# Kernel tuning notes

Measured on AMD Instinct MI355X. Metric: run time of the kernel, lower is better.

The kernel has to match this reference:

```python
import jax, jax.numpy as jnp
import numpy as np

N = 50000      # nodes per graph
E = 1600000    # edges per graph
D_IN = 128
D_HID = 128
D_OUT = 128
D_GF = 128
N_LAYERS = 3   # input->hid, hid->hid (hidden_layer=1), hid->out


def setup_inputs() -> dict:
    key = jax.random.key(0)
    ks = jax.random.split(key, 24)
    inp = {
        "feat_p": jax.random.normal(ks[0], (N, D_IN), jnp.float32),
        "src_p": jax.random.randint(ks[1], (E,), 0, N, jnp.int32),
        "dst_p": jax.random.randint(ks[2], (E,), 0, N, jnp.int32),
        "feat_s": jax.random.normal(ks[3], (N, D_IN), jnp.float32),
        "src_s": jax.random.randint(ks[4], (E,), 0, N, jnp.int32),
        "dst_s": jax.random.randint(ks[5], (E,), 0, N, jnp.int32),
    }
    dims = [(D_IN, D_HID), (D_HID, D_HID), (D_HID, D_OUT)]
    for i, (di, do) in enumerate(dims):
        inp[f"W{i}"] = jax.random.normal(ks[6 + 2 * i], (di, do), jnp.float32) * 0.05
        inp[f"b{i}"] = jnp.zeros((do,), jnp.float32)
    inp["Wr"] = jax.random.normal(ks[14], (D_OUT, D_GF), jnp.float32) * 0.05
    inp["br"] = jnp.zeros((D_GF,), jnp.float32)
    inp["Wm1"] = jax.random.normal(ks[15], (2 * D_GF, D_GF), jnp.float32) * 0.05
    inp["bm1"] = jnp.zeros((D_GF,), jnp.float32)
    inp["Wm2"] = jax.random.normal(ks[16], (D_GF, 1), jnp.float32) * 0.05
    inp["bm2"] = jnp.zeros((1,), jnp.float32)
    return inp


def _gcn_stack(feat, src, dst, layers):
    """Stacked GCN: mean over incoming messages, then linear.
    NOTE: the original SingleGCN never applies its ReLU (bug preserved)."""
    n = feat.shape[0]
    deg = jax.ops.segment_sum(jnp.ones_like(src, feat.dtype), dst, num_segments=n)
    inv_deg = (1.0 / jnp.maximum(deg, 1.0))[:, None]  # [N,1]
    h = feat
    for W, b in layers:
        msg = h[src]                                           # [E,d] gather
        agg = jax.ops.segment_sum(msg, dst, num_segments=n)    # [N,d] scatter-add
        h = (agg * inv_deg) @ W + b                            # mean + linear
    return h


def reference(feat_p, src_p, dst_p, feat_s, src_s, dst_s,
              W0, b0, W1, b1, W2, b2, Wr, br, Wm1, bm1, Wm2, bm2):
    layers = [(W0, b0), (W1, b1), (W2, b2)]
    h_p = _gcn_stack(feat_p, src_p, dst_p, layers)
    h_s = _gcn_stack(feat_s, src_s, dst_s, layers)
    # ReadOut: mean over nodes -> linear -> sigmoid
    g_p = jax.nn.sigmoid(jnp.mean(h_p, axis=0) @ Wr + br)  # [D_GF]
    g_s = jax.nn.sigmoid(jnp.mean(h_s, axis=0) @ Wr + br)
    # Match: concat -> linear -> linear -> sigmoid
    c = jnp.concatenate([g_p, g_s], axis=-1)               # [2*D_GF]
    d = (c @ Wm1 + bm1) @ Wm2 + bm2                        # [1]
    return jax.nn.sigmoid(d)
```

## Files before the change

kernel.cpp:

```cpp
#include <hip/hip_runtime.h>
#include <math.h>

#define D 128


__global__ __launch_bounds__(512) void scan_scatter(
        const int* __restrict__ tgt_p, const int* __restrict__ oth_p,
        const int* __restrict__ tgt_s, const int* __restrict__ oth_s,
        const float* __restrict__ w, float* __restrict__ rep,
        float* __restrict__ sums,
        int E, int N, int HN, int B, int H, float scale) {
    const int b = blockIdx.x, h = blockIdx.y, g = blockIdx.z;
    const int* tgt = g ? tgt_s : tgt_p;
    const int* oth = g ? oth_s : oth_p;
    const float* wg = w ? (w + (size_t)g * N) : nullptr;

    if (!w && b == 0 && h == 0 && g == 0 && threadIdx.x < 16) sums[threadIdx.x] = 0.f;

    extern __shared__ float lds[];
    {
        float4 z = make_float4(0.f, 0.f, 0.f, 0.f);
        float4* l4 = (float4*)lds;
        for (int i = threadIdx.x; i < HN / 4; i += blockDim.x) l4[i] = z;
    }
    __syncthreads();

    const int lo = h * HN;
    const int hi = min(lo + HN, N);
    const unsigned span = (unsigned)(hi - lo);
    int C = (E + B - 1) / B;
    C = (C + 15) & ~15;
    const int e0 = b * C;
    const int e1 = min(e0 + C, E);

    for (int e = e0 + (int)threadIdx.x * 16; e < e1; e += (int)blockDim.x * 16) {
        if (e + 16 <= e1) {
            int idx[16];
            #pragma unroll
            for (int q = 0; q < 4; ++q) {
                int4 t4 = *(const int4*)(tgt + e + 4 * q);
                idx[4 * q + 0] = t4.x; idx[4 * q + 1] = t4.y;
                idx[4 * q + 2] = t4.z; idx[4 * q + 3] = t4.w;
            }
            bool hit[16];
            #pragma unroll
            for (int k = 0; k < 16; ++k) hit[k] = (unsigned)(idx[k] - lo) < span;
            if (wg) {
                int od[16];
                #pragma unroll
                for (int q = 0; q < 4; ++q) {
                    int4 o4 = *(const int4*)(oth + e + 4 * q);
                    od[4 * q + 0] = o4.x; od[4 * q + 1] = o4.y;
                    od[4 * q + 2] = o4.z; od[4 * q + 3] = o4.w;
                }
                float val[16];
                #pragma unroll
                for (int k = 0; k < 16; ++k) val[k] = hit[k] ? wg[od[k]] : 0.f;
                #pragma unroll
                for (int k = 0; k < 16; ++k)
                    if (hit[k]) atomicAdd(&lds[idx[k] - lo], val[k] * scale);
            } else {
                #pragma unroll
                for (int k = 0; k < 16; ++k)
                    if (hit[k]) atomicAdd(&lds[idx[k] - lo], 1.0f);
            }
        } else {
            for (int e2 = e; e2 < e1; ++e2) {
                int t = tgt[e2];
                if ((unsigned)(t - lo) < span) {
                    float v = wg ? wg[oth[e2]] * scale : 1.0f;
                    atomicAdd(&lds[t - lo], v);
                }
            }
        }
    }
    __syncthreads();

    float* dst = rep + (((size_t)g * H + h) * B + b) * HN;
    float4* d4 = (float4*)dst;
    const float4* l4 = (const float4*)lds;
    for (int i = threadIdx.x; i < HN / 4; i += blockDim.x) d4[i] = l4[i];
}

__global__ __launch_bounds__(256) void reduce_inv(
        const float* __restrict__ rep, float* __restrict__ inv,
        int N, int HN, int H, int B) {
    const int lane = threadIdx.x & 63;
    const int s = threadIdx.x >> 6;
    const int i = (blockIdx.x * 64 + lane) * 4;
    const int bps = B >> 2;
    float4 u = make_float4(0.f, 0.f, 0.f, 0.f);
    if (i < 2 * N) {
        int g = (i < N) ? 0 : 1;
        int n = i - g * N;
        int h = n / HN, l = n - h * HN;
        const float* base = rep + (((size_t)g * H + h) * B + (size_t)s * bps) * HN + l;
        #pragma unroll 24
        for (int b = 0; b < bps; b++) {
            float4 v = *(const float4*)(base + (size_t)b * HN);
            u.x += v.x; u.y += v.y; u.z += v.z; u.w += v.w;
        }
    }
    __shared__ float4 sm[256];
    sm[threadIdx.x] = u;
    __syncthreads();
    if (s == 0 && i < 2 * N) {
        float4 a = sm[lane], b4 = sm[64 + lane], c = sm[128 + lane], d = sm[192 + lane];
        float4 r;
        r.x = 1.0f / fmaxf(a.x + b4.x + c.x + d.x, 1.0f);
        r.y = 1.0f / fmaxf(a.y + b4.y + c.y + d.y, 1.0f);
        r.z = 1.0f / fmaxf(a.z + b4.z + c.z + d.z, 1.0f);
        r.w = 1.0f / fmaxf(a.w + b4.w + c.w + d.w, 1.0f);
        *(float4*)(inv + i) = r;
    }
}

__global__ __launch_bounds__(256) void reduce_u(
        const float* __restrict__ rep, const float* __restrict__ inv,
        float* __restrict__ out_u, float* __restrict__ out_w,
        float* __restrict__ sums, int s_idx, int N, int HN, int H, int B) {
    const int lane = threadIdx.x & 63;
    const int s = threadIdx.x >> 6;
    const int i = (blockIdx.x * 64 + lane) * 4;
    const int bps = B >> 2;
    float4 u = make_float4(0.f, 0.f, 0.f, 0.f);
    if (i < 2 * N) {
        int g = (i < N) ? 0 : 1;
        int n = i - g * N;
        int h = n / HN, l = n - h * HN;
        const float* base = rep + (((size_t)g * H + h) * B + (size_t)s * bps) * HN + l;
        #pragma unroll 24
        for (int b = 0; b < bps; b++) {
            float4 v = *(const float4*)(base + (size_t)b * HN);
            u.x += v.x; u.y += v.y; u.z += v.z; u.w += v.w;
        }
    }
    __shared__ float4 sm[256];
    __shared__ float s0[64], s1[64];
    sm[threadIdx.x] = u;
    __syncthreads();
    if (s == 0) {
        float tp = 0.f, ts = 0.f;
        if (i < 2 * N) {
            float4 a = sm[lane], b4 = sm[64 + lane], c = sm[128 + lane], d = sm[192 + lane];
            float4 uu;
            uu.x = a.x + b4.x + c.x + d.x;
            uu.y = a.y + b4.y + c.y + d.y;
            uu.z = a.z + b4.z + c.z + d.z;
            uu.w = a.w + b4.w + c.w + d.w;
            if (out_u) *(float4*)(out_u + i) = uu;
            if (out_w) {
                float4 iv = *(const float4*)(inv + i);
                *(float4*)(out_w + i) =
                    make_float4(uu.x * iv.x, uu.y * iv.y, uu.z * iv.z, uu.w * iv.w);
            }
            float t = uu.x + uu.y + uu.z + uu.w;
            if (i < N) tp = t; else ts = t;
        }
        s0[lane] = tp; s1[lane] = ts;
    }
    __syncthreads();
    if (sums) {
        for (int st = 32; st > 0; st >>= 1) {
            if ((int)threadIdx.x < st) {
                s0[threadIdx.x] += s0[threadIdx.x + st];
                s1[threadIdx.x] += s1[threadIdx.x + st];
            }
            __syncthreads();
        }
        if (threadIdx.x == 0) {
            if (s0[0] != 0.f) atomicAdd(&sums[0 * 2 + s_idx], s0[0]);
            if (s1[0] != 0.f) atomicAdd(&sums[1 * 2 + s_idx], s1[0]);
        }
    }
}

__global__ __launch_bounds__(256) void featsum_kernel(
        const float* __restrict__ feat_p, const float* __restrict__ feat_s,
        const float* __restrict__ u3, float* __restrict__ fpart, int N, int rpb) {
    const int g = blockIdx.y;
    const float* feat = g ? feat_s : feat_p;
    const float* u = u3 + (size_t)g * N;
    const int nb = gridDim.x;
    const int col4 = threadIdx.x & 31;
    const int rgrp = threadIdx.x >> 5;
    const int r0 = blockIdx.x * rpb;
    const int r1 = min(r0 + rpb, N);

    const float4* f4 = (const float4*)feat;
    float4 acc = make_float4(0.f, 0.f, 0.f, 0.f);
    for (int n = r0 + rgrp * 4; n + 3 < r1; n += 32) {
        float4 uu = *(const float4*)(u + n);
        float4 v0 = f4[(size_t)n * 32 + col4];
        float4 v1 = f4[(size_t)(n + 1) * 32 + col4];
        float4 v2 = f4[(size_t)(n + 2) * 32 + col4];
        float4 v3 = f4[(size_t)(n + 3) * 32 + col4];
        acc.x += uu.x * v0.x + uu.y * v1.x + uu.z * v2.x + uu.w * v3.x;
        acc.y += uu.x * v0.y + uu.y * v1.y + uu.z * v2.y + uu.w * v3.y;
        acc.z += uu.x * v0.z + uu.y * v1.z + uu.z * v2.z + uu.w * v3.z;
        acc.w += uu.x * v0.w + uu.y * v1.w + uu.z * v2.w + uu.w * v3.w;
    }
    __shared__ float4 smem[256];
    smem[threadIdx.x] = acc;
    __syncthreads();
    if (rgrp == 0) {
        float4 t = smem[col4];
        #pragma unroll
        for (int k = 1; k < 8; k++) {
            float4 o = smem[k * 32 + col4];
            t.x += o.x; t.y += o.y; t.z += o.z; t.w += o.w;
        }
        float4* dst = (float4*)(fpart + ((size_t)g * nb + blockIdx.x) * 128);
        dst[col4] = t;
    }
}

__global__ __launch_bounds__(256) void fpart_reduce(
        const float* __restrict__ fpart, float* __restrict__ fpart2, int NB) {
    const int b = blockIdx.x, g = blockIdx.y;
    const int j = threadIdx.x & 127, half = threadIdx.x >> 7;
    const int per = NB / 16;
    const int hp = per / 2;
    const float* fp = fpart + ((size_t)(g * NB + b * per + half * hp)) * 128 + j;
    float s = 0.f;
    #pragma unroll 24
    for (int k = 0; k < hp; ++k) s += fp[(size_t)k * 128];
    __shared__ float sm[2][128];
    sm[half][j] = s;
    __syncthreads();
    if (half == 0) fpart2[((size_t)g * 16 + b) * 128 + j] = sm[0][j] + sm[1][j];
}

__global__ __launch_bounds__(512) void final_kernel(
        const float* __restrict__ fpart2,
        const float* __restrict__ sums,
        const float* __restrict__ W0, const float* __restrict__ b0,
        const float* __restrict__ W1, const float* __restrict__ b1,
        const float* __restrict__ W2, const float* __restrict__ b2,
        const float* __restrict__ Wr, const float* __restrict__ br,
        const float* __restrict__ Wm1, const float* __restrict__ bm1,
        const float* __restrict__ Wm2, const float* __restrict__ bm2,
        float* __restrict__ out) {
    __shared__ float x[128];
    __shared__ float part[4][128];
    __shared__ float rvec[256];
    __shared__ float Avec[128], Bvec[128];
    __shared__ float gv[256];
    const int tid = threadIdx.x;
    const int j = tid & 127;
    const int h = tid >> 7;

    auto mv128 = [&](const float* __restrict__ W, float* __restrict__ buf) {
        float p = 0.f;
        const float* Wp = W + (size_t)(h * 32) * 128 + j;
        #pragma unroll
        for (int i = 0; i < 32; ++i) p += buf[h * 32 + i] * Wp[(size_t)i * 128];
        part[h][j] = p;
        __syncthreads();
        if (h == 0) buf[j] = part[0][j] + part[1][j] + part[2][j] + part[3][j];
        __syncthreads();
    };

    if (tid < 256) {
        int g = tid >> 7;
        const float* fp = fpart2 + (size_t)g * 2048 + (tid & 127);
        float rv = 0.f;
        #pragma unroll
        for (int b = 0; b < 16; ++b) rv += fp[(size_t)b * 128];
        rvec[tid] = rv;
    }
    __syncthreads();

    if (tid < 128) x[tid] = b0[tid];
    __syncthreads();
    mv128(W1, x);
    mv128(W2, x);
    if (tid < 128) Avec[tid] = x[tid];
    __syncthreads();
    if (tid < 128) x[tid] = b1[tid];
    __syncthreads();
    mv128(W2, x);
    if (tid < 128) Bvec[tid] = x[tid];
    __syncthreads();

    for (int g = 0; g < 2; ++g) {
        const float s1 = sums[g * 2 + 0];
        const float s2 = sums[g * 2 + 1];
        if (tid < 128) x[tid] = rvec[g * 128 + tid];
        __syncthreads();
        mv128(W0, x);
        mv128(W1, x);
        mv128(W2, x);
        if (tid < 128) x[tid] += s2 * Avec[tid] + s1 * Bvec[tid] + b2[tid];
        __syncthreads();
        mv128(Wr, x);
        if (tid < 128) gv[g * 128 + tid] = 1.0f / (1.0f + expf(-(x[tid] + br[tid])));
        __syncthreads();
    }

    {
        float p = 0.f;
        const float* Wp = Wm1 + (size_t)(h * 64) * 128 + j;
        #pragma unroll
        for (int i = 0; i < 64; ++i) p += gv[h * 64 + i] * Wp[(size_t)i * 128];
        part[h][j] = p;
        __syncthreads();
        if (h == 0)
            part[0][j] = (part[0][j] + part[1][j] + part[2][j] + part[3][j] + bm1[j]) * Wm2[j];
        __syncthreads();
        if (tid < 64) part[0][tid] += part[0][tid + 64];
        __syncthreads();
        if (tid < 32) part[0][tid] += part[0][tid + 32];
        __syncthreads();
        if (tid < 16) part[0][tid] += part[0][tid + 16];
        __syncthreads();
        if (tid < 8) part[0][tid] += part[0][tid + 8];
        __syncthreads();
        if (tid < 4) part[0][tid] += part[0][tid + 4];
        __syncthreads();
        if (tid < 2) part[0][tid] += part[0][tid + 2];
        __syncthreads();
        if (tid == 0) out[0] = 1.0f / (1.0f + expf(-(part[0][0] + part[0][1] + bm2[0])));
    }
}

extern "C" void kernel_launch(void* const* d_in, const int* in_sizes, int n_in,
                              void* d_out, int out_size, void* d_ws, size_t ws_size,
                              hipStream_t stream) {
    const float* feat_p = (const float*)d_in[0];
    const int*   src_p  = (const int*)d_in[1];
    const int*   dst_p  = (const int*)d_in[2];
    const float* feat_s = (const float*)d_in[3];
    const int*   src_s  = (const int*)d_in[4];
    const int*   dst_s  = (const int*)d_in[5];
    const float* W0 = (const float*)d_in[6];
    const float* b0 = (const float*)d_in[7];
    const float* W1 = (const float*)d_in[8];
    const float* b1 = (const float*)d_in[9];
    const float* W2 = (const float*)d_in[10];
    const float* b2 = (const float*)d_in[11];
    const float* Wr = (const float*)d_in[12];
    const float* br = (const float*)d_in[13];
    const float* Wm1 = (const float*)d_in[14];
    const float* bm1 = (const float*)d_in[15];
    const float* Wm2 = (const float*)d_in[16];
    const float* bm2 = (const float*)d_in[17];
    float* out = (float*)d_out;

    const int N = in_sizes[0] / D;
    const int E = in_sizes[1];
    const int N2 = 2 * N;

    const int H = 4;
    int HN = (N + H - 1) / H;
    HN = (HN + 3) & ~3;
    const int NB = 768;
    int rpb = ((N + NB - 1) / NB + 3) & ~3;

    const size_t head = 16 + 4 * (size_t)N2 + (size_t)2 * NB * 128 + 2 * 16 * 128;
    size_t avail = ws_size / sizeof(float);
    int B = 8;
    if (avail > head) {
        size_t bmax = (avail - head) / ((size_t)2 * H * HN);
        if (bmax > 96) bmax = 96;
        B = (int)(bmax & ~(size_t)7);
        if (B < 8) B = 8;
    }

    float* ws     = (float*)d_ws;
    float* sums   = ws;
    float* inv    = ws + 16;
    float* w1     = inv + N2;
    float* w2     = w1 + N2;
    float* u3     = w2 + N2;
    float* fpart  = u3 + N2;
    float* fpart2 = fpart + (size_t)2 * NB * 128;
    float* rep    = fpart2 + 2 * 16 * 128;

    const int BTS = 512;
    const int BT = 256;
    const dim3 sgrid(B, H, 2);
    const size_t lds_bytes = (size_t)HN * sizeof(float);
    const int gQ = (N2 / 4 + 63) / 64;
    const float u0 = 1.0f / (float)N;

    scan_scatter<<<sgrid, BTS, lds_bytes, stream>>>(dst_p, nullptr, dst_s, nullptr,
                                                    nullptr, rep, sums, E, N, HN, B, H, 1.0f);
    reduce_inv<<<gQ, BT, 0, stream>>>(rep, inv, N, HN, H, B);

    scan_scatter<<<sgrid, BTS, lds_bytes, stream>>>(src_p, dst_p, src_s, dst_s,
                                                    inv, rep, sums, E, N, HN, B, H, u0);
    reduce_u<<<gQ, BT, 0, stream>>>(rep, inv, nullptr, w1, sums, 0, N, HN, H, B);

    scan_scatter<<<sgrid, BTS, lds_bytes, stream>>>(src_p, dst_p, src_s, dst_s,
                                                    w1, rep, sums, E, N, HN, B, H, 1.0f);
    reduce_u<<<gQ, BT, 0, stream>>>(rep, inv, nullptr, w2, sums, 1, N, HN, H, B);

    scan_scatter<<<sgrid, BTS, lds_bytes, stream>>>(src_p, dst_p, src_s, dst_s,
                                                    w2, rep, sums, E, N, HN, B, H, 1.0f);
    reduce_u<<<gQ, BT, 0, stream>>>(rep, inv, u3, nullptr, nullptr, 0, N, HN, H, B);

    featsum_kernel<<<dim3(NB, 2), BT, 0, stream>>>(feat_p, feat_s, u3, fpart, N, rpb);
    fpart_reduce<<<dim3(16, 2), BT, 0, stream>>>(fpart, fpart2, NB);

    final_kernel<<<1, 512, 0, stream>>>(fpart2, sums, W0, b0, W1, b1, W2, b2,
                                        Wr, br, Wm1, bm1, Wm2, bm2, out);
}
```

Measured before the change: 288.8 us.

## Fuse all phases into one persistent kernel with software grid barriers

Replaces the eleven separate kernel launches (scatter passes, reductions, feature sum, final MLP) with a single persistent kernel of 512 blocks that runs each phase and separates phases with atomic-counter grid barriers. It fixes the edge-split count at 64 blocks per partition instead of sizing it from workspace, and resizes the reduction and featsum block mappings. The aim is to remove launch gaps and tail effects between the short phases. In exchange it relies on all 512 blocks being co-resident (deadlock risk otherwise) and adds barrier spin cost plus a memset of the counters.

```diff
diff --git a/kernel.cpp b/kernel.cpp
--- a/kernel.cpp
+++ b/kernel.cpp
@@ -2,38 +2,73 @@
 #include <math.h>
 
 #define D 128
-
-
-__global__ __launch_bounds__(512) void scan_scatter(
-        const int* __restrict__ tgt_p, const int* __restrict__ oth_p,
-        const int* __restrict__ tgt_s, const int* __restrict__ oth_s,
-        const float* __restrict__ w, float* __restrict__ rep,
-        float* __restrict__ sums,
-        int E, int N, int HN, int B, int H, float scale) {
-    const int b = blockIdx.x, h = blockIdx.y, g = blockIdx.z;
+#define HQ 4
+#define NBLK 512
+#define BB 64
+
+
+struct Params {
+    const float* feat_p; const int* src_p; const int* dst_p;
+    const float* feat_s; const int* src_s; const int* dst_s;
+    const float *W0, *b0, *W1, *b1, *W2, *b2;
+    const float *Wr, *br, *Wm1, *bm1, *Wm2, *bm2;
+    float* out;
+    int*   bar;
+    float* sums;
+    float* inv;
+    float* w1;
+    float* w2;
+    float* u3;
+    float* fpart;
+    float* fpart2;
+    float* rep;
+    int N, E, HN, NBg;
+    float u0;
+};
+
+__device__ __forceinline__ void gsync(int* bar, int idx) {
+    __syncthreads();
+    if (threadIdx.x == 0) {
+        __threadfence();
+        atomicAdd(&bar[idx], 1);
+        while (__hip_atomic_load(&bar[idx], __ATOMIC_RELAXED,
+                                 __HIP_MEMORY_SCOPE_AGENT) < NBLK)
+            __builtin_amdgcn_s_sleep(2);
+        __threadfence();
+    }
+    __syncthreads();
+}
+
+__device__ __forceinline__ void scan_phase(
+        const Params& p, float* lds,
+        const int* tgt_p, const int* oth_p,
+        const int* tgt_s, const int* oth_s,
+        const float* w, float scale) {
+    const int HN = p.HN, N = p.N, E = p.E;
+    const int id = blockIdx.x;
+    const int b = id % BB;
+    const int h = (id / BB) % HQ;
+    const int g = id / (HQ * BB);
     const int* tgt = g ? tgt_s : tgt_p;
     const int* oth = g ? oth_s : oth_p;
     const float* wg = w ? (w + (size_t)g * N) : nullptr;
 
-    if (!w && b == 0 && h == 0 && g == 0 && threadIdx.x < 16) sums[threadIdx.x] = 0.f;
-
-    extern __shared__ float lds[];
     {
         float4 z = make_float4(0.f, 0.f, 0.f, 0.f);
         float4* l4 = (float4*)lds;
-        for (int i = threadIdx.x; i < HN / 4; i += blockDim.x) l4[i] = z;
+        for (int i = threadIdx.x; i < HN / 4; i += 512) l4[i] = z;
     }
     __syncthreads();
 
     const int lo = h * HN;
     const int hi = min(lo + HN, N);
     const unsigned span = (unsigned)(hi - lo);
-    int C = (E + B - 1) / B;
+    int C = (E + BB - 1) / BB;
     C = (C + 15) & ~15;
     const int e0 = b * C;
     const int e1 = min(e0 + C, E);
 
-    for (int e = e0 + (int)threadIdx.x * 16; e < e1; e += (int)blockDim.x * 16) {
+    for (int e = e0 + (int)threadIdx.x * 16; e < e1; e += 512 * 16) {
         if (e + 16 <= e1) {
             int idx[16];
             #pragma unroll
@@ -76,92 +111,67 @@
     }
     __syncthreads();
 
-    float* dst = rep + (((size_t)g * H + h) * B + b) * HN;
+    float* dst = p.rep + (((size_t)g * HQ + h) * BB + b) * HN;
     float4* d4 = (float4*)dst;
     const float4* l4 = (const float4*)lds;
-    for (int i = threadIdx.x; i < HN / 4; i += blockDim.x) d4[i] = l4[i];
-}
-
-__global__ __launch_bounds__(256) void reduce_inv(
-        const float* __restrict__ rep, float* __restrict__ inv,
-        int N, int HN, int H, int B) {
-    const int lane = threadIdx.x & 63;
-    const int s = threadIdx.x >> 6;
-    const int i = (blockIdx.x * 64 + lane) * 4;
-    const int bps = B >> 2;
+    for (int i = threadIdx.x; i < HN / 4; i += 512) d4[i] = l4[i];
+}
+
+__device__ __forceinline__ void reduce_phase(
+        const Params& p, float* lds, int mode, int s_idx,
+        float* out_u, float* out_w) {
+    const int N = p.N, HN = p.HN;
+    const int lane = threadIdx.x & 127;
+    const int s = threadIdx.x >> 7;
+    const int i = (blockIdx.x * 128 + lane) * 4;
+    const int bps = BB >> 2;
     float4 u = make_float4(0.f, 0.f, 0.f, 0.f);
     if (i < 2 * N) {
         int g = (i < N) ? 0 : 1;
         int n = i - g * N;
         int h = n / HN, l = n - h * HN;
-        const float* base = rep + (((size_t)g * H + h) * B + (size_t)s * bps) * HN + l;
-        #pragma unroll 24
+        const float* base = p.rep + (((size_t)g * HQ + h) * BB + (size_t)s * bps) * HN + l;
+        #pragma unroll 16
         for (int b = 0; b < bps; b++) {
             float4 v = *(const float4*)(base + (size_t)b * HN);
             u.x += v.x; u.y += v.y; u.z += v.z; u.w += v.w;
         }
     }
-    __shared__ float4 sm[256];
-    sm[threadIdx.x] = u;
-    __syncthreads();
-    if (s == 0 && i < 2 * N) {
-        float4 a = sm[lane], b4 = sm[64 + lane], c = sm[128 + lane], d = sm[192 + lane];
-        float4 r;
-        r.x = 1.0f / fmaxf(a.x + b4.x + c.x + d.x, 1.0f);
-        r.y = 1.0f / fmaxf(a.y + b4.y + c.y + d.y, 1.0f);
-        r.z = 1.0f / fmaxf(a.z + b4.z + c.z + d.z, 1.0f);
-        r.w = 1.0f / fmaxf(a.w + b4.w + c.w + d.w, 1.0f);
-        *(float4*)(inv + i) = r;
-    }
-}
-
-__global__ __launch_bounds__(256) void reduce_u(
-        const float* __restrict__ rep, const float* __restrict__ inv,
-        float* __restrict__ out_u, float* __restrict__ out_w,
-        float* __restrict__ sums, int s_idx, int N, int HN, int H, int B) {
-    const int lane = threadIdx.x & 63;
-    const int s = threadIdx.x >> 6;
-    const int i = (blockIdx.x * 64 + lane) * 4;
-    const int bps = B >> 2;
-    float4 u = make_float4(0.f, 0.f, 0.f, 0.f);
-    if (i < 2 * N) {
-        int g = (i < N) ? 0 : 1;
-        int n = i - g * N;
-        int h = n / HN, l = n - h * HN;
-        const float* base = rep + (((size_t)g * H + h) * B + (size_t)s * bps) * HN + l;
-        #pragma unroll 24
-        for (int b = 0; b < bps; b++) {
-            float4 v = *(const float4*)(base + (size_t)b * HN);
-            u.x += v.x; u.y += v.y; u.z += v.z; u.w += v.w;
-        }
-    }
-    __shared__ float4 sm[256];
-    __shared__ float s0[64], s1[64];
+    float4* sm = (float4*)lds;
+    float* s0 = lds + 2048;
+    float* s1 = lds + 2176;
     sm[threadIdx.x] = u;
     __syncthreads();
     if (s == 0) {
         float tp = 0.f, ts = 0.f;
         if (i < 2 * N) {
-            float4 a = sm[lane], b4 = sm[64 + lane], c = sm[128 + lane], d = sm[192 + lane];
+            float4 a = sm[lane], b4 = sm[128 + lane], c = sm[256 + lane], d = sm[384 + lane];
             float4 uu;
             uu.x = a.x + b4.x + c.x + d.x;
             uu.y = a.y + b4.y + c.y + d.y;
             uu.z = a.z + b4.z + c.z + d.z;
             uu.w = a.w + b4.w + c.w + d.w;
-            if (out_u) *(float4*)(out_u + i) = uu;
-            if (out_w) {
-                float4 iv = *(const float4*)(inv + i);
-                *(float4*)(out_w + i) =
-                    make_float4(uu.x * iv.x, uu.y * iv.y, uu.z * iv.z, uu.w * iv.w);
-            }
-            float t = uu.x + uu.y + uu.z + uu.w;
-            if (i < N) tp = t; else ts = t;
+            if (mode == 0) {
+                float4 r;
+                r.x = 1.0f / fmaxf(uu.x, 1.0f); r.y = 1.0f / fmaxf(uu.y, 1.0f);
+                r.z = 1.0f / fmaxf(uu.z, 1.0f); r.w = 1.0f / fmaxf(uu.w, 1.0f);
+                *(float4*)(p.inv + i) = r;
+            } else {
+                if (out_u) *(float4*)(out_u + i) = uu;
+                if (out_w) {
+                    float4 iv = *(const float4*)(p.inv + i);
+                    *(float4*)(out_w + i) =
+                        make_float4(uu.x * iv.x, uu.y * iv.y, uu.z * iv.z, uu.w * iv.w);
+                }
+                float t = uu.x + uu.y + uu.z + uu.w;
+                if (i < N) tp = t; else ts = t;
+            }
         }
         s0[lane] = tp; s1[lane] = ts;
     }
     __syncthreads();
-    if (sums) {
-        for (int st = 32; st > 0; st >>= 1) {
+    if (mode == 1 && s_idx >= 0) {
+        for (int st = 64; st > 0; st >>= 1) {
             if ((int)threadIdx.x < st) {
                 s0[threadIdx.x] += s0[threadIdx.x + st];
                 s1[threadIdx.x] += s1[threadIdx.x + st];
@@ -169,27 +179,28 @@
             __syncthreads();
         }
         if (threadIdx.x == 0) {
-            if (s0[0] != 0.f) atomicAdd(&sums[0 * 2 + s_idx], s0[0]);
-            if (s1[0] != 0.f) atomicAdd(&sums[1 * 2 + s_idx], s1[0]);
-        }
-    }
-}
-
-__global__ __launch_bounds__(256) void featsum_kernel(
-        const float* __restrict__ feat_p, const float* __restrict__ feat_s,
-        const float* __restrict__ u3, float* __restrict__ fpart, int N, int rpb) {
-    const int g = blockIdx.y;
-    const float* feat = g ? feat_s : feat_p;
-    const float* u = u3 + (size_t)g * N;
-    const int nb = gridDim.x;
+            if (s0[0] != 0.f) atomicAdd(&p.sums[0 * 2 + s_idx], s0[0]);
+            if (s1[0] != 0.f) atomicAdd(&p.sums[1 * 2 + s_idx], s1[0]);
+        }
+    }
+}
+
+__device__ __forceinline__ void featsum_phase(const Params& p, float* lds) {
+    const int NBg = p.NBg;
+    const int id = blockIdx.x;
+    const int g = id / NBg;
+    const int bg = id - g * NBg;
+    const float* feat = g ? p.feat_s : p.feat_p;
+    const float* u = p.u3 + (size_t)g * p.N;
+    const int rpb = ((p.N + NBg - 1) / NBg + 3) & ~3;
+    const int r0 = bg * rpb;
+    const int r1 = min(r0 + rpb, p.N);
     const int col4 = threadIdx.x & 31;
-    const int rgrp = threadIdx.x >> 5;
-    const int r0 = blockIdx.x * rpb;
-    const int r1 = min(r0 + rpb, N);
+    const int rg = threadIdx.x >> 5;
 
     const float4* f4 = (const float4*)feat;
     float4 acc = make_float4(0.f, 0.f, 0.f, 0.f);
-    for (int n = r0 + rgrp * 4; n + 3 < r1; n += 32) {
+    for (int n = r0 + rg * 4; n + 3 < r1; n += 64) {
         float4 uu = *(const float4*)(u + n);
         float4 v0 = f4[(size_t)n * 32 + col4];
         float4 v1 = f4[(size_t)(n + 1) * 32 + col4];
@@ -200,70 +211,63 @@
         acc.z += uu.x * v0.z + uu.y * v1.z + uu.z * v2.z + uu.w * v3.z;
         acc.w += uu.x * v0.w + uu.y * v1.w + uu.z * v2.w + uu.w * v3.w;
     }
-    __shared__ float4 smem[256];
+    float4* smem = (float4*)lds;
     smem[threadIdx.x] = acc;
     __syncthreads();
-    if (rgrp == 0) {
+    if (rg == 0) {
         float4 t = smem[col4];
         #pragma unroll
-        for (int k = 1; k < 8; k++) {
+        for (int k = 1; k < 16; k++) {
             float4 o = smem[k * 32 + col4];
             t.x += o.x; t.y += o.y; t.z += o.z; t.w += o.w;
         }
-        float4* dst = (float4*)(fpart + ((size_t)g * nb + blockIdx.x) * 128);
+        float4* dst = (float4*)(p.fpart + ((size_t)g * NBg + bg) * 128);
         dst[col4] = t;
     }
 }
 
-__global__ __launch_bounds__(256) void fpart_reduce(
-        const float* __restrict__ fpart, float* __restrict__ fpart2, int NB) {
-    const int b = blockIdx.x, g = blockIdx.y;
-    const int j = threadIdx.x & 127, half = threadIdx.x >> 7;
-    const int per = NB / 16;
-    const int hp = per / 2;
-    const float* fp = fpart + ((size_t)(g * NB + b * per + half * hp)) * 128 + j;
+__device__ __forceinline__ void fpart2_phase(const Params& p, float* lds) {
+    if (blockIdx.x >= 32) return;
+    const int g = blockIdx.x >> 4, b = blockIdx.x & 15;
+    const int per = p.NBg / 16;
+    const int sl = per / 4;
+    const int j = threadIdx.x & 127, seg = threadIdx.x >> 7;
+    const float* fp = p.fpart + ((size_t)(g * p.NBg + b * per + seg * sl)) * 128 + j;
     float s = 0.f;
-    #pragma unroll 24
-    for (int k = 0; k < hp; ++k) s += fp[(size_t)k * 128];
-    __shared__ float sm[2][128];
-    sm[half][j] = s;
-    __syncthreads();
-    if (half == 0) fpart2[((size_t)g * 16 + b) * 128 + j] = sm[0][j] + sm[1][j];
-}
-
-__global__ __launch_bounds__(512) void final_kernel(
-        const float* __restrict__ fpart2,
-        const float* __restrict__ sums,
-        const float* __restrict__ W0, const float* __restrict__ b0,
-        const float* __restrict__ W1, const float* __restrict__ b1,
-        const float* __restrict__ W2, const float* __restrict__ b2,
-        const float* __restrict__ Wr, const float* __restrict__ br,
-        const float* __restrict__ Wm1, const float* __restrict__ bm1,
-        const float* __restrict__ Wm2, const float* __restrict__ bm2,
-        float* __restrict__ out) {
-    __shared__ float x[128];
-    __shared__ float part[4][128];
-    __shared__ float rvec[256];
-    __shared__ float Avec[128], Bvec[128];
-    __shared__ float gv[256];
+    #pragma unroll 4
+    for (int k = 0; k < sl; ++k) s += fp[(size_t)k * 128];
+    lds[seg * 128 + j] = s;
+    __syncthreads();
+    if (seg == 0)
+        p.fpart2[((size_t)g * 16 + b) * 128 + j] =
+            lds[j] + lds[128 + j] + lds[256 + j] + lds[384 + j];
+}
+
+__device__ __forceinline__ void final_phase(const Params& p, float* lds) {
+    float* x    = lds;
+    float* part = lds + 128;
+    float* rvec = lds + 640;
+    float* Avec = lds + 896;
+    float* Bvec = lds + 1024;
+    float* gv   = lds + 1152;
     const int tid = threadIdx.x;
     const int j = tid & 127;
     const int h = tid >> 7;
 
     auto mv128 = [&](const float* __restrict__ W, float* __restrict__ buf) {
-        float p = 0.f;
+        float pp = 0.f;
         const float* Wp = W + (size_t)(h * 32) * 128 + j;
         #pragma unroll
-        for (int i = 0; i < 32; ++i) p += buf[h * 32 + i] * Wp[(size_t)i * 128];
-        part[h][j] = p;
-        __syncthreads();
-        if (h == 0) buf[j] = part[0][j] + part[1][j] + part[2][j] + part[3][j];
+        for (int i = 0; i < 32; ++i) pp += buf[h * 32 + i] * Wp[(size_t)i * 128];
+        part[h * 128 + j] = pp;
+        __syncthreads();
+        if (h == 0) buf[j] = part[j] + part[128 + j] + part[256 + j] + part[384 + j];
         __syncthreads();
     };
 
     if (tid < 256) {
         int g = tid >> 7;
-        const float* fp = fpart2 + (size_t)g * 2048 + (tid & 127);
+        const float* fp = p.fpart2 + (size_t)g * 2048 + (tid & 127);
         float rv = 0.f;
         #pragma unroll
         for (int b = 0; b < 16; ++b) rv += fp[(size_t)b * 128];
@@ -271,138 +275,122 @@
     }
     __syncthreads();
 
-    if (tid < 128) x[tid] = b0[tid];
-    __syncthreads();
-    mv128(W1, x);
-    mv128(W2, x);
+    if (tid < 128) x[tid] = p.b0[tid];
+    __syncthreads();
+    mv128(p.W1, x);
+    mv128(p.W2, x);
     if (tid < 128) Avec[tid] = x[tid];
     __syncthreads();
-    if (tid < 128) x[tid] = b1[tid];
-    __syncthreads();
-    mv128(W2, x);
+    if (tid < 128) x[tid] = p.b1[tid];
+    __syncthreads();
+    mv128(p.W2, x);
     if (tid < 128) Bvec[tid] = x[tid];
     __syncthreads();
 
     for (int g = 0; g < 2; ++g) {
-        const float s1 = sums[g * 2 + 0];
-        const float s2 = sums[g * 2 + 1];
+        const float s1 = p.sums[g * 2 + 0];
+        const float s2 = p.sums[g * 2 + 1];
         if (tid < 128) x[tid] = rvec[g * 128 + tid];
         __syncthreads();
-        mv128(W0, x);
-        mv128(W1, x);
-        mv128(W2, x);
-        if (tid < 128) x[tid] += s2 * Avec[tid] + s1 * Bvec[tid] + b2[tid];
-        __syncthreads();
-        mv128(Wr, x);
-        if (tid < 128) gv[g * 128 + tid] = 1.0f / (1.0f + expf(-(x[tid] + br[tid])));
+        mv128(p.W0, x);
+        mv128(p.W1, x);
+        mv128(p.W2, x);
+        if (tid < 128) x[tid] += s2 * Avec[tid] + s1 * Bvec[tid] + p.b2[tid];
+        __syncthreads();
+        mv128(p.Wr, x);
+        if (tid < 128) gv[g * 128 + tid] = 1.0f / (1.0f + expf(-(x[tid] + p.br[tid])));
         __syncthreads();
     }
 
     {
-        float p = 0.f;
-        const float* Wp = Wm1 + (size_t)(h * 64) * 128 + j;
+        float pp = 0.f;
+        const float* Wp = p.Wm1 + (size_t)(h * 64) * 128 + j;
         #pragma unroll
-        for (int i = 0; i < 64; ++i) p += gv[h * 64 + i] * Wp[(size_t)i * 128];
-        part[h][j] = p;
+        for (int i = 0; i < 64; ++i) pp += gv[h * 64 + i] * Wp[(size_t)i * 128];
+        part[h * 128 + j] = pp;
         __syncthreads();
         if (h == 0)
-            part[0][j] = (part[0][j] + part[1][j] + part[2][j] + part[3][j] + bm1[j]) * Wm2[j];
-        __syncthreads();
-        if (tid < 64) part[0][tid] += part[0][tid + 64];
-        __syncthreads();
-        if (tid < 32) part[0][tid] += part[0][tid + 32];
-        __syncthreads();
-        if (tid < 16) part[0][tid] += part[0][tid + 16];
-        __syncthreads();
-        if (tid < 8) part[0][tid] += part[0][tid + 8];
-        __syncthreads();
-        if (tid < 4) part[0][tid] += part[0][tid + 4];
-        __syncthreads();
-        if (tid < 2) part[0][tid] += part[0][tid + 2];
-        __syncthreads();
-        if (tid == 0) out[0] = 1.0f / (1.0f + expf(-(part[0][0] + part[0][1] + bm2[0])));
-    }
+            part[j] = (part[j] + part[128 + j] + part[256 + j] + part[384 + j] + p.bm1[j]) * p.Wm2[j];
+        __syncthreads();
+        for (int st = 64; st > 1; st >>= 1) {
+            if (tid < st) part[tid] += part[tid + st];
+            __syncthreads();
+        }
+        if (tid == 0)
+            p.out[0] = 1.0f / (1.0f + expf(-(part[0] + part[1] + p.bm2[0])));
+    }
+}
+
+__global__ __launch_bounds__(512, 4) void fused_kernel(Params p) {
+    extern __shared__ float lds[];
+    int* bar = p.bar;
+
+    scan_phase(p, lds, p.dst_p, nullptr, p.dst_s, nullptr, nullptr, 1.0f);
+    gsync(bar, 0);
+    reduce_phase(p, lds, 0, -1, nullptr, nullptr);
+    gsync(bar, 1);
+    scan_phase(p, lds, p.src_p, p.dst_p, p.src_s, p.dst_s, p.inv, p.u0);
+    gsync(bar, 2);
+    reduce_phase(p, lds, 1, 0, nullptr, p.w1);
+    gsync(bar, 3);
+    scan_phase(p, lds, p.src_p, p.dst_p, p.src_s, p.dst_s, p.w1, 1.0f);
+    gsync(bar, 4);
+    reduce_phase(p, lds, 1, 1, nullptr, p.w2);
+    gsync(bar, 5);
+    scan_phase(p, lds, p.src_p, p.dst_p, p.src_s, p.dst_s, p.w2, 1.0f);
+    gsync(bar, 6);
+    reduce_phase(p, lds, 1, -1, p.u3, nullptr);
+    gsync(bar, 7);
+    featsum_phase(p, lds);
+    gsync(bar, 8);
+    fpart2_phase(p, lds);
+    gsync(bar, 9);
+    if (blockIdx.x == 0) final_phase(p, lds);
 }
 
 extern "C" void kernel_launch(void* const* d_in, const int* in_sizes, int n_in,
                               void* d_out, int out_size, void* d_ws, size_t ws_size,
                               hipStream_t stream) {
-    const float* feat_p = (const float*)d_in[0];
-    const int*   src_p  = (const int*)d_in[1];
-    const int*   dst_p  = (const int*)d_in[2];
-    const float* feat_s = (const float*)d_in[3];
-    const int*   src_s  = (const int*)d_in[4];
-    const int*   dst_s  = (const int*)d_in[5];
-    const float* W0 = (const float*)d_in[6];
-    const float* b0 = (const float*)d_in[7];
-    const float* W1 = (const float*)d_in[8];
-    const float* b1 = (const float*)d_in[9];
-    const float* W2 = (const float*)d_in[10];
-    const float* b2 = (const float*)d_in[11];
-    const float* Wr = (const float*)d_in[12];
-    const float* br = (const float*)d_in[13];
-    const float* Wm1 = (const float*)d_in[14];
-    const float* bm1 = (const float*)d_in[15];
-    const float* Wm2 = (const float*)d_in[16];
-    const float* bm2 = (const float*)d_in[17];
-    float* out = (float*)d_out;
-
     const int N = in_sizes[0] / D;
     const int E = in_sizes[1];
     const int N2 = 2 * N;
 
-    const int H = 4;
-    int HN = (N + H - 1) / H;
+    int HN = (N + HQ - 1) / HQ;
     HN = (HN + 3) & ~3;
-    const int NB = 768;
-    int rpb = ((N + NB - 1) / NB + 3) & ~3;
-
-    const size_t head = 16 + 4 * (size_t)N2 + (size_t)2 * NB * 128 + 2 * 16 * 128;
-    size_t avail = ws_size / sizeof(float);
-    int B = 8;
-    if (avail > head) {
-        size_t bmax = (avail - head) / ((size_t)2 * H * HN);
-        if (bmax > 96) bmax = 96;
-        B = (int)(bmax & ~(size_t)7);
-        if (B < 8) B = 8;
-    }
+    const int NBg = NBLK / 2;
 
     float* ws     = (float*)d_ws;
-    float* sums   = ws;
-    float* inv    = ws + 16;
+    int*   bar    = (int*)ws;
+    float* sums   = ws + 32;
+    float* inv    = ws + 48;
     float* w1     = inv + N2;
     float* w2     = w1 + N2;
     float* u3     = w2 + N2;
     float* fpart  = u3 + N2;
-    float* fpart2 = fpart + (size_t)2 * NB * 128;
+    float* fpart2 = fpart + (size_t)2 * NBg * 128;
     float* rep    = fpart2 + 2 * 16 * 128;
 
-    const int BTS = 512;
-    const int BT = 256;
-    const dim3 sgrid(B, H, 2);
-    const size_t lds_bytes = (size_t)HN * sizeof(float);
-    const int gQ = (N2 / 4 + 63) / 64;
-    const float u0 = 1.0f / (float)N;
-
-    scan_scatter<<<sgrid, BTS, lds_bytes, stream>>>(dst_p, nullptr, dst_s, nullptr,
-                                                    nullptr, rep, sums, E, N, HN, B, H, 1.0f);
-    reduce_inv<<<gQ, BT, 0, stream>>>(rep, inv, N, HN, H, B);
-
-    scan_scatter<<<sgrid, BTS, lds_bytes, stream>>>(src_p, dst_p, src_s, dst_s,
-                                                    inv, rep, sums, E, N, HN, B, H, u0);
-    reduce_u<<<gQ, BT, 0, stream>>>(rep, inv, nullptr, w1, sums, 0, N, HN, H, B);
-
-    scan_scatter<<<sgrid, BTS, lds_bytes, stream>>>(src_p, dst_p, src_s, dst_s,
-                                                    w1, rep, sums, E, N, HN, B, H, 1.0f);
-    reduce_u<<<gQ, BT, 0, stream>>>(rep, inv, nullptr, w2, sums, 1, N, HN, H, B);
-
-    scan_scatter<<<sgrid, BTS, lds_bytes, stream>>>(src_p, dst_p, src_s, dst_s,
-                                                    w2, rep, sums, E, N, HN, B, H, 1.0f);
-    reduce_u<<<gQ, BT, 0, stream>>>(rep, inv, u3, nullptr, nullptr, 0, N, HN, H, B);
-
-    featsum_kernel<<<dim3(NB, 2), BT, 0, stream>>>(feat_p, feat_s, u3, fpart, N, rpb);
-    fpart_reduce<<<dim3(16, 2), BT, 0, stream>>>(fpart, fpart2, NB);
-
-    final_kernel<<<1, 512, 0, stream>>>(fpart2, sums, W0, b0, W1, b1, W2, b2,
-                                        Wr, br, Wm1, bm1, Wm2, bm2, out);
-}
+    hipMemsetAsync(d_ws, 0, 48 * sizeof(float), stream);
+
+    Params p;
+    p.feat_p = (const float*)d_in[0];
+    p.src_p  = (const int*)d_in[1];
+    p.dst_p  = (const int*)d_in[2];
+    p.feat_s = (const float*)d_in[3];
+    p.src_s  = (const int*)d_in[4];
+    p.dst_s  = (const int*)d_in[5];
+    p.W0 = (const float*)d_in[6];  p.b0 = (const float*)d_in[7];
+    p.W1 = (const float*)d_in[8];  p.b1 = (const float*)d_in[9];
+    p.W2 = (const float*)d_in[10]; p.b2 = (const float*)d_in[11];
+    p.Wr = (const float*)d_in[12]; p.br = (const float*)d_in[13];
+    p.Wm1 = (const float*)d_in[14]; p.bm1 = (const float*)d_in[15];
+    p.Wm2 = (const float*)d_in[16]; p.bm2 = (const float*)d_in[17];
+    p.out = (float*)d_out;
+    p.bar = bar; p.sums = sums; p.inv = inv; p.w1 = w1; p.w2 = w2; p.u3 = u3;
+    p.fpart = fpart; p.fpart2 = fpart2; p.rep = rep;
+    p.N = N; p.E = E; p.HN = HN; p.NBg = NBg;
+    p.u0 = 1.0f / (float)N;
+
+    const unsigned lds_bytes = (unsigned)(HN * sizeof(float));
+    fused_kernel<<<NBLK, 512, lds_bytes, stream>>>(p);
+}
```

After: 889.9 us. 3.08x slower.

## Fix scatter grid, widen blocks to 1024 threads, fold feature partial reduction into atomics

Applied to the files above, without the earlier changes.

The edge-scatter kernel now uses a fixed grid of 64 edge chunks by 4 node ranges by 2 graphs, with 1024-thread blocks each handling 8 edges per thread. Previously the number of chunks was derived from workspace size, up to 96, with 512 threads and 16 edges per thread. The featsum kernel drops from 768 to 256 blocks and accumulates its partials directly into 16 bins with global atomics, which removes the separate fpart_reduce launch. Zeroing of the sums and bins moves into the first scatter launch. The trade-offs are a different amount of replicated LDS output per reduction pass and possible atomic contention on the bins.

```diff
diff --git a/kernel.cpp b/kernel.cpp
--- a/kernel.cpp
+++ b/kernel.cpp
@@ -2,66 +2,61 @@
 #include <math.h>
 
 #define D 128
-
-
-__global__ __launch_bounds__(512) void scan_scatter(
+#define HQ 4
+#define BB 64
+
+
+__global__ __launch_bounds__(1024, 8) void scan_scatter(
         const int* __restrict__ tgt_p, const int* __restrict__ oth_p,
         const int* __restrict__ tgt_s, const int* __restrict__ oth_s,
         const float* __restrict__ w, float* __restrict__ rep,
-        float* __restrict__ sums,
-        int E, int N, int HN, int B, int H, float scale) {
+        float* __restrict__ zbase, int zcount,
+        int E, int N, int HN, float scale) {
     const int b = blockIdx.x, h = blockIdx.y, g = blockIdx.z;
     const int* tgt = g ? tgt_s : tgt_p;
     const int* oth = g ? oth_s : oth_p;
     const float* wg = w ? (w + (size_t)g * N) : nullptr;
 
-    if (!w && b == 0 && h == 0 && g == 0 && threadIdx.x < 16) sums[threadIdx.x] = 0.f;
+    if (zbase && b == 0 && h == 0 && g == 0)
+        for (int i = threadIdx.x; i < zcount; i += 1024) zbase[i] = 0.f;
 
     extern __shared__ float lds[];
     {
         float4 z = make_float4(0.f, 0.f, 0.f, 0.f);
         float4* l4 = (float4*)lds;
-        for (int i = threadIdx.x; i < HN / 4; i += blockDim.x) l4[i] = z;
+        for (int i = threadIdx.x; i < HN / 4; i += 1024) l4[i] = z;
     }
     __syncthreads();
 
     const int lo = h * HN;
     const int hi = min(lo + HN, N);
     const unsigned span = (unsigned)(hi - lo);
-    int C = (E + B - 1) / B;
-    C = (C + 15) & ~15;
+    int C = (E + BB - 1) / BB;
+    C = (C + 7) & ~7;
     const int e0 = b * C;
     const int e1 = min(e0 + C, E);
 
-    for (int e = e0 + (int)threadIdx.x * 16; e < e1; e += (int)blockDim.x * 16) {
-        if (e + 16 <= e1) {
-            int idx[16];
+    for (int e = e0 + (int)threadIdx.x * 8; e < e1; e += 1024 * 8) {
+        if (e + 8 <= e1) {
+            int4 ta = *(const int4*)(tgt + e);
+            int4 tb = *(const int4*)(tgt + e + 4);
+            int idx[8] = {ta.x, ta.y, ta.z, ta.w, tb.x, tb.y, tb.z, tb.w};
+            bool hit[8];
             #pragma unroll
-            for (int q = 0; q < 4; ++q) {
-                int4 t4 = *(const int4*)(tgt + e + 4 * q);
-                idx[4 * q + 0] = t4.x; idx[4 * q + 1] = t4.y;
-                idx[4 * q + 2] = t4.z; idx[4 * q + 3] = t4.w;
-            }
-            bool hit[16];
-            #pragma unroll
-            for (int k = 0; k < 16; ++k) hit[k] = (unsigned)(idx[k] - lo) < span;
+            for (int k = 0; k < 8; ++k) hit[k] = (unsigned)(idx[k] - lo) < span;
             if (wg) {
-                int od[16];
+                int4 oa = *(const int4*)(oth + e);
+                int4 ob = *(const int4*)(oth + e + 4);
+                int od[8] = {oa.x, oa.y, oa.z, oa.w, ob.x, ob.y, ob.z, ob.w};
+                float val[8];
                 #pragma unroll
-                for (int q = 0; q < 4; ++q) {
-                    int4 o4 = *(const int4*)(oth + e + 4 * q);
-                    od[4 * q + 0] = o4.x; od[4 * q + 1] = o4.y;
-                    od[4 * q + 2] = o4.z; od[4 * q + 3] = o4.w;
-                }
-                float val[16];
+                for (int k = 0; k < 8; ++k) val[k] = hit[k] ? wg[od[k]] : 0.f;
                 #pragma unroll
-                for (int k = 0; k < 16; ++k) val[k] = hit[k] ? wg[od[k]] : 0.f;
-                #pragma unroll
-                for (int k = 0; k < 16; ++k)
+                for (int k = 0; k < 8; ++k)
                     if (hit[k]) atomicAdd(&lds[idx[k] - lo], val[k] * scale);
             } else {
                 #pragma unroll
-                for (int k = 0; k < 16; ++k)
+                for (int k = 0; k < 8; ++k)
                     if (hit[k]) atomicAdd(&lds[idx[k] - lo], 1.0f);
             }
         } else {
@@ -76,26 +71,26 @@
     }
     __syncthreads();
 
-    float* dst = rep + (((size_t)g * H + h) * B + b) * HN;
+    float* dst = rep + (((size_t)g * HQ + h) * BB + b) * HN;
     float4* d4 = (float4*)dst;
     const float4* l4 = (const float4*)lds;
-    for (int i = threadIdx.x; i < HN / 4; i += blockDim.x) d4[i] = l4[i];
+    for (int i = threadIdx.x; i < HN / 4; i += 1024) d4[i] = l4[i];
 }
 
 __global__ __launch_bounds__(256) void reduce_inv(
         const float* __restrict__ rep, float* __restrict__ inv,
-        int N, int HN, int H, int B) {
+        int N, int HN) {
     const int lane = threadIdx.x & 63;
     const int s = threadIdx.x >> 6;
     const int i = (blockIdx.x * 64 + lane) * 4;
-    const int bps = B >> 2;
+    const int bps = BB >> 2;
     float4 u = make_float4(0.f, 0.f, 0.f, 0.f);
     if (i < 2 * N) {
         int g = (i < N) ? 0 : 1;
         int n = i - g * N;
         int h = n / HN, l = n - h * HN;
-        const float* base = rep + (((size_t)g * H + h) * B + (size_t)s * bps) * HN + l;
-        #pragma unroll 24
+        const float* base = rep + (((size_t)g * HQ + h) * BB + (size_t)s * bps) * HN + l;
+        #pragma unroll 16
         for (int b = 0; b < bps; b++) {
             float4 v = *(const float4*)(base + (size_t)b * HN);
             u.x += v.x; u.y += v.y; u.z += v.z; u.w += v.w;
@@ -118,18 +113,18 @@
 __global__ __launch_bounds__(256) void reduce_u(
         const float* __restrict__ rep, const float* __restrict__ inv,
         float* __restrict__ out_u, float* __restrict__ out_w,
-        float* __restrict__ sums, int s_idx, int N, int HN, int H, int B) {
+        float* __restrict__ sums, int s_idx, int N, int HN) {
     const int lane = threadIdx.x & 63;
     const int s = threadIdx.x >> 6;
     const int i = (blockIdx.x * 64 + lane) * 4;
-    const int bps = B >> 2;
+    const int bps = BB >> 2;
     float4 u = make_float4(0.f, 0.f, 0.f, 0.f);
     if (i < 2 * N) {
         int g = (i < N) ? 0 : 1;
         int n = i - g * N;
         int h = n / HN, l = n - h * HN;
-        const float* base = rep + (((size_t)g * H + h) * B + (size_t)s * bps) * HN + l;
-        #pragma unroll 24
+        const float* base = rep + (((size_t)g * HQ + h) * BB + (size_t)s * bps) * HN + l;
+        #pragma unroll 16
         for (int b = 0; b < bps; b++) {
             float4 v = *(const float4*)(base + (size_t)b * HN);
             u.x += v.x; u.y += v.y; u.z += v.z; u.w += v.w;
@@ -177,11 +172,11 @@
 
 __global__ __launch_bounds__(256) void featsum_kernel(
         const float* __restrict__ feat_p, const float* __restrict__ feat_s,
-        const float* __restrict__ u3, float* __restrict__ fpart, int N, int rpb) {
+        const float* __restrict__ u3, float* __restrict__ fpart2,
+        int N, int rpb) {
     const int g = blockIdx.y;
     const float* feat = g ? feat_s : feat_p;
     const float* u = u3 + (size_t)g * N;
-    const int nb = gridDim.x;
     const int col4 = threadIdx.x & 31;
     const int rgrp = threadIdx.x >> 5;
     const int r0 = blockIdx.x * rpb;
@@ -210,25 +205,12 @@
             float4 o = smem[k * 32 + col4];
             t.x += o.x; t.y += o.y; t.z += o.z; t.w += o.w;
         }
-        float4* dst = (float4*)(fpart + ((size_t)g * nb + blockIdx.x) * 128);
-        dst[col4] = t;
-    }
-}
-
-__global__ __launch_bounds__(256) void fpart_reduce(
-        const float* __restrict__ fpart, float* __restrict__ fpart2, int NB) {
-    const int b = blockIdx.x, g = blockIdx.y;
-    const int j = threadIdx.x & 127, half = threadIdx.x >> 7;
-    const int per = NB / 16;
-    const int hp = per / 2;
-    const float* fp = fpart + ((size_t)(g * NB + b * per + half * hp)) * 128 + j;
-    float s = 0.f;
-    #pragma unroll 24
-    for (int k = 0; k < hp; ++k) s += fp[(size_t)k * 128];
-    __shared__ float sm[2][128];
-    sm[half][j] = s;
-    __syncthreads();
-    if (half == 0) fpart2[((size_t)g * 16 + b) * 128 + j] = sm[0][j] + sm[1][j];
+        float* dst = fpart2 + ((size_t)g * 16 + (blockIdx.x & 15)) * 128 + col4 * 4;
+        atomicAdd(dst + 0, t.x);
+        atomicAdd(dst + 1, t.y);
+        atomicAdd(dst + 2, t.z);
+        atomicAdd(dst + 3, t.w);
+    }
 }
 
 __global__ __launch_bounds__(512) void final_kernel(
@@ -351,57 +333,47 @@
     const int E = in_sizes[1];
     const int N2 = 2 * N;
 
-    const int H = 4;
-    int HN = (N + H - 1) / H;
+    int HN = (N + HQ - 1) / HQ;
     HN = (HN + 3) & ~3;
-    const int NB = 768;
-    int rpb = ((N + NB - 1) / NB + 3) & ~3;
-
-    const size_t head = 16 + 4 * (size_t)N2 + (size_t)2 * NB * 128 + 2 * 16 * 128;
-    size_t avail = ws_size / sizeof(float);
-    int B = 8;
-    if (avail > head) {
-        size_t bmax = (avail - head) / ((size_t)2 * H * HN);
-        if (bmax > 96) bmax = 96;
-        B = (int)(bmax & ~(size_t)7);
-        if (B < 8) B = 8;
-    }
+    const int FB = 256;
+    const int rpb = (((N + FB - 1) / FB) + 3) & ~3;
 
     float* ws     = (float*)d_ws;
     float* sums   = ws;
-    float* inv    = ws + 16;
+    float* fpart2 = ws + 16;
+    float* inv    = fpart2 + 2 * 16 * 128;
     float* w1     = inv + N2;
     float* w2     = w1 + N2;
     float* u3     = w2 + N2;
-    float* fpart  = u3 + N2;
-    float* fpart2 = fpart + (size_t)2 * NB * 128;
-    float* rep    = fpart2 + 2 * 16 * 128;
-
-    const int BTS = 512;
-    const int BT = 256;
-    const dim3 sgrid(B, H, 2);
+    float* rep    = u3 + N2;
+
+    const dim3 sgrid(BB, HQ, 2);
     const size_t lds_bytes = (size_t)HN * sizeof(float);
     const int gQ = (N2 / 4 + 63) / 64;
     const float u0 = 1.0f / (float)N;
-
-    scan_scatter<<<sgrid, BTS, lds_bytes, stream>>>(dst_p, nullptr, dst_s, nullptr,
-                                                    nullptr, rep, sums, E, N, HN, B, H, 1.0f);
-    reduce_inv<<<gQ, BT, 0, stream>>>(rep, inv, N, HN, H, B);
-
-    scan_scatter<<<sgrid, BTS, lds_bytes, stream>>>(src_p, dst_p, src_s, dst_s,
-                                                    inv, rep, sums, E, N, HN, B, H, u0);
-    reduce_u<<<gQ, BT, 0, stream>>>(rep, inv, nullptr, w1, sums, 0, N, HN, H, B);
-
-    scan_scatter<<<sgrid, BTS, lds_bytes, stream>>>(src_p, dst_p, src_s, dst_s,
-                                                    w1, rep, sums, E, N, HN, B, H, 1.0f);
-    reduce_u<<<gQ, BT, 0, stream>>>(rep, inv, nullptr, w2, sums, 1, N, HN, H, B);
-
-    scan_scatter<<<sgrid, BTS, lds_bytes, stream>>>(src_p, dst_p, src_s, dst_s,
-                                                    w2, rep, sums, E, N, HN, B, H, 1.0f);
-    reduce_u<<<gQ, BT, 0, stream>>>(rep, inv, u3, nullptr, nullptr, 0, N, HN, H, B);
-
-    featsum_kernel<<<dim3(NB, 2), BT, 0, stream>>>(feat_p, feat_s, u3, fpart, N, rpb);
-    fpart_reduce<<<dim3(16, 2), BT, 0, stream>>>(fpart, fpart2, NB);
+    const int zcount = 16 + 2 * 16 * 128;
+
+    scan_scatter<<<sgrid, 1024, lds_bytes, stream>>>(dst_p, nullptr, dst_s, nullptr,
+                                                     nullptr, rep, sums, zcount,
+                                                     E, N, HN, 1.0f);
+    reduce_inv<<<gQ, 256, 0, stream>>>(rep, inv, N, HN);
+
+    scan_scatter<<<sgrid, 1024, lds_bytes, stream>>>(src_p, dst_p, src_s, dst_s,
+                                                     inv, rep, nullptr, 0,
+                                                     E, N, HN, u0);
+    reduce_u<<<gQ, 256, 0, stream>>>(rep, inv, nullptr, w1, sums, 0, N, HN);
+
+    scan_scatter<<<sgrid, 1024, lds_bytes, stream>>>(src_p, dst_p, src_s, dst_s,
+                                                     w1, rep, nullptr, 0,
+                                                     E, N, HN, 1.0f);
+    reduce_u<<<gQ, 256, 0, stream>>>(rep, inv, nullptr, w2, sums, 1, N, HN);
+
+    scan_scatter<<<sgrid, 1024, lds_bytes, stream>>>(src_p, dst_p, src_s, dst_s,
+                                                     w2, rep, nullptr, 0,
+                                                     E, N, HN, 1.0f);
+    reduce_u<<<gQ, 256, 0, stream>>>(rep, inv, u3, nullptr, nullptr, 0, N, HN);
+
+    featsum_kernel<<<dim3(FB, 2), 256, 0, stream>>>(feat_p, feat_s, u3, fpart2, N, rpb);
 
     final_kernel<<<1, 512, 0, stream>>>(fpart2, sums, W0, b0, W1, b1, W2, b2,
                                         Wr, br, Wm1, bm1, Wm2, bm2, out);
```

New measurement: 279.5 us. 1.03x faster.
